# Optimization experiments

Measured on AMD Instinct MI355X. Metric: run time of the kernel, lower is better.

Reference implementation:

```python
import jax, jax.numpy as jnp
import numpy as np

B, T, D, H = 4, 2048, 1024, 16
HD = D // H  # head_dim = 64

def setup_inputs() -> dict:
    key = jax.random.key(0)
    k1, k2, k3 = jax.random.split(key, 3)
    x = jax.random.normal(k1, (B, T, D), dtype=jnp.float32)
    w_qkv = jax.random.normal(k2, (D, 3 * D), dtype=jnp.float32) * (D ** -0.5)
    b_qkv = jnp.zeros((3 * D,), dtype=jnp.float32)
    w_proj = jax.random.normal(k3, (D, D), dtype=jnp.float32) * (D ** -0.5)
    b_proj = jnp.zeros((D,), dtype=jnp.float32)
    return {"x": x, "w_qkv": w_qkv, "b_qkv": b_qkv, "w_proj": w_proj, "b_proj": b_proj}

def reference(x, w_qkv, b_qkv, w_proj, b_proj):
    b, t, d = x.shape
    scale = HD ** -0.5
    qkv = x @ w_qkv + b_qkv                          # [B,T,3D]
    qkv = qkv.reshape(b, t, 3, H, HD)
    qkv = jnp.transpose(qkv, (2, 0, 3, 1, 4))        # [3,B,H,T,HD]
    q, k, v = qkv[0], qkv[1], qkv[2]
    att = jnp.einsum("bhqd,bhkd->bhqk", q, k) * scale  # [B,H,T,T]
    mask = jnp.tril(jnp.ones((t, t), dtype=att.dtype))[None, None]
    att = att * mask + (1.0 - mask) * (-1e9)
    att = jax.nn.softmax(att, axis=-1)
    # dropout inactive (training=False)
    y = jnp.einsum("bhqk,bhkd->bhqd", att, v)        # [B,H,T,HD]
    y = jnp.transpose(y, (0, 2, 1, 3)).reshape(b, t, d)
    return y @ w_proj + b_proj
```

## Files before the change

kernel.cpp:

```cpp
#include <hip/hip_runtime.h>
#include <hip/hip_bf16.h>

typedef unsigned short u16;
typedef short short8 __attribute__((ext_vector_type(8)));
typedef short bf16x4 __attribute__((ext_vector_type(4)));
typedef float f32x4 __attribute__((ext_vector_type(4)));
typedef float f32x16 __attribute__((ext_vector_type(16)));

#define B_SZ 4
#define T_SEQ 2048
#define DMODEL 1024
#define NH 16
#define HD 64
#define QKV_ELEMS 8388608ull
#define QSCALE (0.125f * 1.44269504f)

__device__ __forceinline__ u16 f2bf(float f) {
    __hip_bfloat16 h = __float2bfloat16(f);
    return __builtin_bit_cast(u16, h);
}

__device__ __forceinline__ void gload16(const void* g, void* l) {
    __builtin_amdgcn_global_load_lds(
        (const __attribute__((address_space(1))) unsigned int*)g,
        (__attribute__((address_space(3))) unsigned int*)l, 16, 0, 0);
}

__global__ __launch_bounds__(256) void cast_x_kernel(
    const float4* __restrict__ x, u16* __restrict__ xb)
{
    const int i = blockIdx.x * 256 + threadIdx.x;
    const float4 v = x[i];
    union { u16 u[4]; uint2 d; } p;
    p.u[0] = f2bf(v.x); p.u[1] = f2bf(v.y); p.u[2] = f2bf(v.z); p.u[3] = f2bf(v.w);
    *(uint2*)(xb + (size_t)i * 4) = p.d;
}

__global__ __launch_bounds__(256) void tcast_kernel(
    const float* __restrict__ w, u16* __restrict__ wt, int K, int N)
{
    const int n = blockIdx.x * 256 + threadIdx.x;
    const int k0 = blockIdx.y * 256;
    for (int kk = 0; kk < 256; kk += 8) {
        short8 o;
#pragma unroll
        for (int e = 0; e < 8; ++e)
            o[e] = (short)f2bf(w[(size_t)(k0 + kk + e) * N + n]);
        *(short8*)&wt[(size_t)n * K + k0 + kk] = o;
    }
}

template <int EPI>
__global__ __launch_bounds__(256) void gemm_kernel(
    const u16* __restrict__ A, const u16* __restrict__ Bt,
    const float* __restrict__ bias, void* __restrict__ outp)
{
    __shared__ u16 As[128 * 64];
    __shared__ u16 Bs[128 * 64];
    const int tid = threadIdx.x;
    const int l = tid & 63;
    const int w = tid >> 6;
    const int wm = w >> 1, wn = w & 1;
    const int m0 = blockIdx.y * 128, n0 = blockIdx.x * 128;
    const int srow = l >> 3;
    const int sch  = (l & 7) ^ srow;
    const int fr = l & 15, fq = l >> 4;

    f32x4 acc[4][4] = {};

    for (int k0 = 0; k0 < 1024; k0 += 64) {
        __syncthreads();
#pragma unroll
        for (int ii = 0; ii < 4; ++ii) {
            const int row = w * 32 + ii * 8;
            gload16(&A[(size_t)(m0 + row + srow) * 1024 + k0 + sch * 8], &As[row * 64]);
            gload16(&Bt[(size_t)(n0 + row + srow) * 1024 + k0 + sch * 8], &Bs[row * 64]);
        }
        __syncthreads();
#pragma unroll
        for (int ks = 0; ks < 2; ++ks) {
            short8 af[4], bf[4];
#pragma unroll
            for (int t = 0; t < 4; ++t) {
                const int ar = wm * 64 + t * 16 + fr;
                af[t] = *(const short8*)&As[ar * 64 + (((ks * 4 + fq) ^ (l & 7)) << 3)];
                const int br = wn * 64 + t * 16 + fr;
                bf[t] = *(const short8*)&Bs[br * 64 + (((ks * 4 + fq) ^ (l & 7)) << 3)];
            }
#pragma unroll
            for (int mt = 0; mt < 4; ++mt)
#pragma unroll
                for (int nt = 0; nt < 4; ++nt)
                    acc[mt][nt] = __builtin_amdgcn_mfma_f32_16x16x32_bf16(
                        af[mt], bf[nt], acc[mt][nt], 0, 0, 0);
        }
    }

    if (EPI == 0) {
        u16* qkv = (u16*)outp;
#pragma unroll
        for (int nt = 0; nt < 4; ++nt) {
            const int n = n0 + wn * 64 + nt * 16 + fr;
            const float bs = bias[n];
            const int which = n >> 10, hh = (n >> 6) & 15, d = n & 63;
            if (which == 2) {
                u16* dst = qkv + 2 * QKV_ELEMS;
#pragma unroll
                for (int mt = 0; mt < 4; ++mt) {
                    const int m = m0 + wm * 64 + mt * 16 + fq * 4;
                    const int bb = m >> 11, t = m & 2047;
                    bf16x4 ov;
#pragma unroll
                    for (int r = 0; r < 4; ++r) ov[r] = (short)f2bf(acc[mt][nt][r] + bs);
                    *(bf16x4*)&dst[(((size_t)(bb * NH + hh)) * HD + d) * T_SEQ + t] = ov;
                }
            } else {
                const float scl = (which == 0) ? QSCALE : 1.0f;
                u16* dst = qkv + (size_t)which * QKV_ELEMS + (size_t)hh * T_SEQ * HD + d;
#pragma unroll
                for (int mt = 0; mt < 4; ++mt)
#pragma unroll
                    for (int r = 0; r < 4; ++r) {
                        const int m = m0 + wm * 64 + mt * 16 + fq * 4 + r;
                        const int bb = m >> 11, t = m & 2047;
                        dst[(size_t)bb * (NH * T_SEQ * HD) + (size_t)t * HD] =
                            f2bf((acc[mt][nt][r] + bs) * scl);
                    }
            }
        }
    } else {
        float* C = (float*)outp;
#pragma unroll
        for (int nt = 0; nt < 4; ++nt) {
            const int n = n0 + wn * 64 + nt * 16 + fr;
            const float bs = bias[n];
#pragma unroll
            for (int mt = 0; mt < 4; ++mt)
#pragma unroll
                for (int r = 0; r < 4; ++r) {
                    const int m = m0 + wm * 64 + mt * 16 + fq * 4 + r;
                    C[(size_t)m * DMODEL + n] = acc[mt][nt][r] + bs;
                }
        }
    }
}

__global__ __launch_bounds__(256, 4) void attn_kernel(
    const u16* __restrict__ q, const u16* __restrict__ k,
    const u16* __restrict__ vT, u16* __restrict__ y)
{
    __shared__ u16 Ks[2][64 * 64];
    __shared__ u16 Vs[2][64 * 64];

    static const int PI[16] = {15, 14, 13, 12, 8, 9, 10, 11, 4, 5, 6, 7, 3, 2, 1, 0};
    const int bx = blockIdx.x;
    const int qi = PI[bx >> 6];
    const int bhpos = bx & 63;
    const int hh = bhpos & 15;
    const int bb = bhpos >> 4;
    const int q0 = qi * 128;

    const size_t hbase = ((size_t)(bb * NH + hh)) * T_SEQ * HD;
    const u16* qb = q + hbase;
    const u16* kb = k + hbase;
    const u16* vTb = vT + hbase;

    const int tid = threadIdx.x;
    const int l = tid & 63;
    const int w = tid >> 6;
    const int qn = l & 31;
    const int h = l >> 5;
    const int srow = l >> 3;
    const int sch = (l & 7) ^ srow;

    u16* Qstage = &Ks[0][0];

#pragma unroll
    for (int ii = 0; ii < 4; ++ii) {
        const int row = w * 32 + ii * 8;
        gload16(&qb[(size_t)(q0 + row + srow) * HD + sch * 8], &Qstage[row * 64]);
    }
    {
        const int row = w * 16, row2 = w * 16 + 8;
        gload16(&vTb[(size_t)(row + srow) * T_SEQ + sch * 8], &Vs[0][row * 64]);
        gload16(&vTb[(size_t)(row2 + srow) * T_SEQ + sch * 8], &Vs[0][row2 * 64]);
    }
    __syncthreads();

    short8 qf[4];
    {
        const int qrow = w * 32 + qn;
#pragma unroll
        for (int k16 = 0; k16 < 4; ++k16)
            qf[k16] = *(const short8*)
                &Qstage[qrow * 64 + (((k16 * 2 + h) ^ (qrow & 7)) << 3)];
    }
    __syncthreads();

    {
        const int row = w * 16, row2 = w * 16 + 8;
        gload16(&kb[(size_t)(row + srow) * HD + sch * 8], &Ks[0][row * 64]);
        gload16(&kb[(size_t)(row2 + srow) * HD + sch * 8], &Ks[0][row2 * 64]);
    }

    const int q0w = q0 + w * 32;
    float l_run = 0.f;
    f32x16 o_acc[2] = {};

    const int nkt = 2 * (qi + 1);
    for (int kt = 0; kt < nkt; ++kt) {
        __syncthreads();
        if (kt + 1 < nkt) {
            const int nb = (kt + 1) & 1;
            const int jj = (kt + 1) * 64;
            const int row = w * 16, row2 = w * 16 + 8;
            gload16(&kb[(size_t)(jj + row + srow) * HD + sch * 8],
                    &Ks[nb][row * 64]);
            gload16(&kb[(size_t)(jj + row2 + srow) * HD + sch * 8],
                    &Ks[nb][row2 * 64]);
            gload16(&vTb[(size_t)(row + srow) * T_SEQ + jj + sch * 8],
                    &Vs[nb][row * 64]);
            gload16(&vTb[(size_t)(row2 + srow) * T_SEQ + jj + sch * 8],
                    &Vs[nb][row2 * 64]);
        }
        const int buf = kt & 1;
        const int j0 = kt * 64;

        if (j0 > q0w + 31) continue;
        const int njt = (j0 + 32 <= q0w + 31) ? 2 : 1;

        f32x16 st[2];
#pragma unroll
        for (int jt = 0; jt < 2; ++jt) {
            if (jt >= njt) continue;
            f32x16 s;
#pragma unroll
            for (int r = 0; r < 16; ++r) s[r] = -16.f;
#pragma unroll
            for (int k16 = 0; k16 < 4; ++k16) {
                const int jrow = jt * 32 + qn;
                const short8 kf = *(const short8*)
                    &Ks[buf][jrow * 64 + (((k16 * 2 + h) ^ (jrow & 7)) << 3)];
                s = __builtin_amdgcn_mfma_f32_32x32x16_bf16(kf, qf[k16], s, 0, 0, 0);
            }
            st[jt] = s;
        }

        const int qg = q0w + qn;
#pragma unroll
        for (int jt = 0; jt < 2; ++jt) {
            if (jt >= njt) continue;
            const bool needMask = (j0 + jt * 32 + 31) > q0w;
            if (needMask) {
#pragma unroll
                for (int r = 0; r < 16; ++r) {
                    const int jg = j0 + jt * 32 + (r & 3) + 8 * (r >> 2) + 4 * h;
                    if (jg > qg) st[jt][r] = -1e30f;
                }
            }
        }

        float ls = 0.f;
#pragma unroll
        for (int jt = 0; jt < 2; ++jt) {
            if (jt >= njt) continue;
            float s0 = 0.f, s1 = 0.f, s2 = 0.f, s3 = 0.f;
#pragma unroll
            for (int r = 0; r < 16; r += 4) {
                float p0 = exp2f(st[jt][r]);
                float p1 = exp2f(st[jt][r + 1]);
                float p2 = exp2f(st[jt][r + 2]);
                float p3 = exp2f(st[jt][r + 3]);
                st[jt][r] = p0; st[jt][r + 1] = p1;
                st[jt][r + 2] = p2; st[jt][r + 3] = p3;
                s0 += p0; s1 += p1; s2 += p2; s3 += p3;
            }
            ls += (s0 + s1) + (s2 + s3);
        }
        ls += __shfl_xor(ls, 32);
        l_run += ls;

#pragma unroll
        for (int jt = 0; jt < 2; ++jt) {
            if (jt >= njt) continue;
#pragma unroll
            for (int g = 0; g < 4; ++g) {
                bf16x4 pk;
#pragma unroll
                for (int e = 0; e < 4; ++e) pk[e] = (short)f2bf(st[jt][g * 4 + e]);
#pragma unroll
                for (int dt = 0; dt < 2; ++dt) {
                    const int drow = dt * 32 + qn;
                    const bf16x4 vf = *(const bf16x4*)
                        &Vs[buf][drow * 64 +
                                 (((jt * 4 + g) ^ (drow & 7)) << 3) + h * 4];
                    o_acc[dt] = __builtin_amdgcn_mfma_f32_32x32x8bf16_1k(
                        vf, pk, o_acc[dt], 0, 0, 0);
                }
            }
        }
    }

    const float inv = 1.f / l_run;
    const int t = q0w + qn;
    u16* yrow = y + ((size_t)(bb * T_SEQ + t)) * DMODEL + hh * HD;
#pragma unroll
    for (int dt = 0; dt < 2; ++dt)
#pragma unroll
        for (int g = 0; g < 4; ++g) {
            bf16x4 ov;
#pragma unroll
            for (int e = 0; e < 4; ++e)
                ov[e] = (short)f2bf(o_acc[dt][g * 4 + e] * inv);
            *(bf16x4*)&yrow[dt * 32 + g * 8 + h * 4] = ov;
        }
}

extern "C" void kernel_launch(void* const* d_in, const int* in_sizes, int n_in,
                              void* d_out, int out_size, void* d_ws, size_t ws_size,
                              hipStream_t stream) {
    const float* x      = (const float*)d_in[0];
    const float* w_qkv  = (const float*)d_in[1];
    const float* b_qkv  = (const float*)d_in[2];
    const float* w_proj = (const float*)d_in[3];
    const float* b_proj = (const float*)d_in[4];
    float* out = (float*)d_out;

    u16* xb  = (u16*)d_ws;
    u16* wqT = xb + 8388608;
    u16* wpT = wqT + 3145728;
    u16* qkv = wpT + 1048576;
    u16* yb  = qkv + 3 * QKV_ELEMS;

    cast_x_kernel<<<8192, 256, 0, stream>>>((const float4*)x, xb);
    tcast_kernel<<<dim3(12, 4), 256, 0, stream>>>(w_qkv, wqT, 1024, 3072);
    tcast_kernel<<<dim3(4, 4), 256, 0, stream>>>(w_proj, wpT, 1024, 1024);
    gemm_kernel<0><<<dim3(24, 64), 256, 0, stream>>>(xb, wqT, b_qkv, (void*)qkv);
    attn_kernel<<<dim3(1024), 256, 0, stream>>>(
        qkv, qkv + QKV_ELEMS, qkv + 2 * QKV_ELEMS, yb);
    gemm_kernel<1><<<dim3(8, 64), 256, 0, stream>>>(yb, wpT, b_proj, (void*)out);
}
```

Baseline: 326.1 us.

## Balance causal attention work by pairing short and long query tiles with split-K merge

Each attention block now takes a share of a paired short and long query tile. Part 0 computes the short tile in full and then the first half of the long tile's keys. Part 1 computes the rest of the long tile's keys. The partial outputs and row sums go to scratch buffers. An atomic flag decides which block merges them and writes the final row. The aim is to give all 1024 blocks about the same work, removing the causal tail imbalance. The cost is a memset launch, extra global traffic for the partials, and bf16 rounding of the partial outputs.

```diff
diff --git a/kernel.cpp b/kernel.cpp
--- a/kernel.cpp
+++ b/kernel.cpp
@@ -147,18 +147,19 @@
 
 __global__ __launch_bounds__(256, 4) void attn_kernel(
     const u16* __restrict__ q, const u16* __restrict__ k,
-    const u16* __restrict__ vT, u16* __restrict__ y)
+    const u16* __restrict__ vT, u16* __restrict__ y,
+    u16* __restrict__ po, float* __restrict__ pl, unsigned* __restrict__ flg)
 {
     __shared__ u16 Ks[2][64 * 64];
     __shared__ u16 Vs[2][64 * 64];
-
-    static const int PI[16] = {15, 14, 13, 12, 8, 9, 10, 11, 4, 5, 6, 7, 3, 2, 1, 0};
+    __shared__ unsigned who;
+
     const int bx = blockIdx.x;
-    const int qi = PI[bx >> 6];
-    const int bhpos = bx & 63;
-    const int hh = bhpos & 15;
-    const int bb = bhpos >> 4;
-    const int q0 = qi * 128;
+    const int part_id = bx >> 9;
+    const int pr = (bx >> 6) & 7;
+    const int hh = (bx & 7) | (((bx >> 3) & 1) << 3);
+    const int bb = (bx >> 4) & 3;
+    const int pairG = bx & 511;
 
     const size_t hbase = ((size_t)(bb * NH + hh)) * T_SEQ * HD;
     const u16* qb = q + hbase;
@@ -175,145 +176,200 @@
 
     u16* Qstage = &Ks[0][0];
 
-#pragma unroll
-    for (int ii = 0; ii < 4; ++ii) {
-        const int row = w * 32 + ii * 8;
-        gload16(&qb[(size_t)(q0 + row + srow) * HD + sch * 8], &Qstage[row * 64]);
+    auto span = [&](const int q0, const int kt0, const int ktN,
+                    f32x16 (&o_acc)[2], float& l_run) {
+        __syncthreads();
+
+#pragma unroll
+        for (int ii = 0; ii < 4; ++ii) {
+            const int row = w * 32 + ii * 8;
+            gload16(&qb[(size_t)(q0 + row + srow) * HD + sch * 8], &Qstage[row * 64]);
+        }
+        {
+            const int row = w * 16, row2 = w * 16 + 8;
+            gload16(&vTb[(size_t)(row + srow) * T_SEQ + kt0 * 64 + sch * 8],
+                    &Vs[kt0 & 1][row * 64]);
+            gload16(&vTb[(size_t)(row2 + srow) * T_SEQ + kt0 * 64 + sch * 8],
+                    &Vs[kt0 & 1][row2 * 64]);
+        }
+        __syncthreads();
+
+        short8 qf[4];
+        {
+            const int qrow = w * 32 + qn;
+#pragma unroll
+            for (int k16 = 0; k16 < 4; ++k16)
+                qf[k16] = *(const short8*)
+                    &Qstage[qrow * 64 + (((k16 * 2 + h) ^ (qrow & 7)) << 3)];
+        }
+        __syncthreads();
+
+        {
+            const int row = w * 16, row2 = w * 16 + 8;
+            gload16(&kb[(size_t)(kt0 * 64 + row + srow) * HD + sch * 8],
+                    &Ks[kt0 & 1][row * 64]);
+            gload16(&kb[(size_t)(kt0 * 64 + row2 + srow) * HD + sch * 8],
+                    &Ks[kt0 & 1][row2 * 64]);
+        }
+
+        const int q0w = q0 + w * 32;
+
+        for (int kt = kt0; kt < ktN; ++kt) {
+            __syncthreads();
+            if (kt + 1 < ktN) {
+                const int nb = (kt + 1) & 1;
+                const int jj = (kt + 1) * 64;
+                const int row = w * 16, row2 = w * 16 + 8;
+                gload16(&kb[(size_t)(jj + row + srow) * HD + sch * 8],
+                        &Ks[nb][row * 64]);
+                gload16(&kb[(size_t)(jj + row2 + srow) * HD + sch * 8],
+                        &Ks[nb][row2 * 64]);
+                gload16(&vTb[(size_t)(row + srow) * T_SEQ + jj + sch * 8],
+                        &Vs[nb][row * 64]);
+                gload16(&vTb[(size_t)(row2 + srow) * T_SEQ + jj + sch * 8],
+                        &Vs[nb][row2 * 64]);
+            }
+            const int buf = kt & 1;
+            const int j0 = kt * 64;
+
+            if (j0 > q0w + 31) continue;
+            const int njt = (j0 + 32 <= q0w + 31) ? 2 : 1;
+
+            f32x16 st[2];
+#pragma unroll
+            for (int jt = 0; jt < 2; ++jt) {
+                if (jt >= njt) continue;
+                f32x16 s;
+#pragma unroll
+                for (int r = 0; r < 16; ++r) s[r] = -16.f;
+#pragma unroll
+                for (int k16 = 0; k16 < 4; ++k16) {
+                    const int jrow = jt * 32 + qn;
+                    const short8 kf = *(const short8*)
+                        &Ks[buf][jrow * 64 + (((k16 * 2 + h) ^ (jrow & 7)) << 3)];
+                    s = __builtin_amdgcn_mfma_f32_32x32x16_bf16(kf, qf[k16], s, 0, 0, 0);
+                }
+                st[jt] = s;
+            }
+
+            const int qg = q0w + qn;
+#pragma unroll
+            for (int jt = 0; jt < 2; ++jt) {
+                if (jt >= njt) continue;
+                const bool needMask = (j0 + jt * 32 + 31) > q0w;
+                if (needMask) {
+#pragma unroll
+                    for (int r = 0; r < 16; ++r) {
+                        const int jg = j0 + jt * 32 + (r & 3) + 8 * (r >> 2) + 4 * h;
+                        if (jg > qg) st[jt][r] = -1e30f;
+                    }
+                }
+            }
+
+            float ls = 0.f;
+#pragma unroll
+            for (int jt = 0; jt < 2; ++jt) {
+                if (jt >= njt) continue;
+                float s0 = 0.f, s1 = 0.f, s2 = 0.f, s3 = 0.f;
+#pragma unroll
+                for (int r = 0; r < 16; r += 4) {
+                    float p0 = exp2f(st[jt][r]);
+                    float p1 = exp2f(st[jt][r + 1]);
+                    float p2 = exp2f(st[jt][r + 2]);
+                    float p3 = exp2f(st[jt][r + 3]);
+                    st[jt][r] = p0; st[jt][r + 1] = p1;
+                    st[jt][r + 2] = p2; st[jt][r + 3] = p3;
+                    s0 += p0; s1 += p1; s2 += p2; s3 += p3;
+                }
+                ls += (s0 + s1) + (s2 + s3);
+            }
+            ls += __shfl_xor(ls, 32);
+            l_run += ls;
+
+#pragma unroll
+            for (int jt = 0; jt < 2; ++jt) {
+                if (jt >= njt) continue;
+#pragma unroll
+                for (int g = 0; g < 4; ++g) {
+                    bf16x4 pk;
+#pragma unroll
+                    for (int e = 0; e < 4; ++e) pk[e] = (short)f2bf(st[jt][g * 4 + e]);
+#pragma unroll
+                    for (int dt = 0; dt < 2; ++dt) {
+                        const int drow = dt * 32 + qn;
+                        const bf16x4 vf = *(const bf16x4*)
+                            &Vs[buf][drow * 64 +
+                                     (((jt * 4 + g) ^ (drow & 7)) << 3) + h * 4];
+                        o_acc[dt] = __builtin_amdgcn_mfma_f32_32x32x8bf16_1k(
+                            vf, pk, o_acc[dt], 0, 0, 0);
+                    }
+                }
+            }
+        }
+    };
+
+    auto writeY = [&](const int q0, f32x16 (&o)[2], const float lt) {
+        const float inv = 1.f / lt;
+        const int t = q0 + w * 32 + qn;
+        u16* yrow = y + ((size_t)(bb * T_SEQ + t)) * DMODEL + hh * HD;
+#pragma unroll
+        for (int dt = 0; dt < 2; ++dt)
+#pragma unroll
+            for (int g = 0; g < 4; ++g) {
+                bf16x4 ov;
+#pragma unroll
+                for (int e = 0; e < 4; ++e)
+                    ov[e] = (short)f2bf(o[dt][g * 4 + e] * inv);
+                *(bf16x4*)&yrow[dt * 32 + g * 8 + h * 4] = ov;
+            }
+    };
+
+    const int qip = 15 - pr;
+    f32x16 ob[2] = {};
+    float lb = 0.f;
+
+    if (part_id == 0) {
+        f32x16 oa[2] = {};
+        float la = 0.f;
+        span(pr * 128, 0, 2 * pr + 2, oa, la);
+        writeY(pr * 128, oa, la);
+        span(qip * 128, 0, 15 - 2 * pr, ob, lb);
+    } else {
+        span(qip * 128, 15 - 2 * pr, 32 - 2 * pr, ob, lb);
     }
+
     {
-        const int row = w * 16, row2 = w * 16 + 8;
-        gload16(&vTb[(size_t)(row + srow) * T_SEQ + sch * 8], &Vs[0][row * 64]);
-        gload16(&vTb[(size_t)(row2 + srow) * T_SEQ + sch * 8], &Vs[0][row2 * 64]);
+        unsigned* s32 = (unsigned*)(po + (size_t)(pairG * 2 + part_id) * 8192);
+#pragma unroll
+        for (int dt = 0; dt < 2; ++dt)
+#pragma unroll
+            for (int r = 0; r < 16; r += 2) {
+                const unsigned pk = (unsigned)f2bf(ob[dt][r]) |
+                                    ((unsigned)f2bf(ob[dt][r + 1]) << 16);
+                s32[(dt * 8 + (r >> 1)) * 256 + tid] = pk;
+            }
+        pl[(size_t)(pairG * 2 + part_id) * 256 + tid] = lb;
+        __threadfence();
+        __syncthreads();
+        if (tid == 0) who = atomicAdd(&flg[pairG], 1u);
+        __syncthreads();
+        if (who == 1) {
+            __threadfence();
+            const unsigned* o32 = (const unsigned*)
+                (po + (size_t)(pairG * 2 + (1 - part_id)) * 8192);
+            const float lo = pl[(size_t)(pairG * 2 + (1 - part_id)) * 256 + tid];
+            const float lt = lb + lo;
+#pragma unroll
+            for (int dt = 0; dt < 2; ++dt)
+#pragma unroll
+                for (int r = 0; r < 16; r += 2) {
+                    const unsigned v = o32[(dt * 8 + (r >> 1)) * 256 + tid];
+                    ob[dt][r]     += __builtin_bit_cast(float, v << 16);
+                    ob[dt][r + 1] += __builtin_bit_cast(float, v & 0xffff0000u);
+                }
+            writeY(qip * 128, ob, lt);
+        }
     }
-    __syncthreads();
-
-    short8 qf[4];
-    {
-        const int qrow = w * 32 + qn;
-#pragma unroll
-        for (int k16 = 0; k16 < 4; ++k16)
-            qf[k16] = *(const short8*)
-                &Qstage[qrow * 64 + (((k16 * 2 + h) ^ (qrow & 7)) << 3)];
-    }
-    __syncthreads();
-
-    {
-        const int row = w * 16, row2 = w * 16 + 8;
-        gload16(&kb[(size_t)(row + srow) * HD + sch * 8], &Ks[0][row * 64]);
-        gload16(&kb[(size_t)(row2 + srow) * HD + sch * 8], &Ks[0][row2 * 64]);
-    }
-
-    const int q0w = q0 + w * 32;
-    float l_run = 0.f;
-    f32x16 o_acc[2] = {};
-
-    const int nkt = 2 * (qi + 1);
-    for (int kt = 0; kt < nkt; ++kt) {
-        __syncthreads();
-        if (kt + 1 < nkt) {
-            const int nb = (kt + 1) & 1;
-            const int jj = (kt + 1) * 64;
-            const int row = w * 16, row2 = w * 16 + 8;
-            gload16(&kb[(size_t)(jj + row + srow) * HD + sch * 8],
-                    &Ks[nb][row * 64]);
-            gload16(&kb[(size_t)(jj + row2 + srow) * HD + sch * 8],
-                    &Ks[nb][row2 * 64]);
-            gload16(&vTb[(size_t)(row + srow) * T_SEQ + jj + sch * 8],
-                    &Vs[nb][row * 64]);
-            gload16(&vTb[(size_t)(row2 + srow) * T_SEQ + jj + sch * 8],
-                    &Vs[nb][row2 * 64]);
-        }
-        const int buf = kt & 1;
-        const int j0 = kt * 64;
-
-        if (j0 > q0w + 31) continue;
-        const int njt = (j0 + 32 <= q0w + 31) ? 2 : 1;
-
-        f32x16 st[2];
-#pragma unroll
-        for (int jt = 0; jt < 2; ++jt) {
-            if (jt >= njt) continue;
-            f32x16 s;
-#pragma unroll
-            for (int r = 0; r < 16; ++r) s[r] = -16.f;
-#pragma unroll
-            for (int k16 = 0; k16 < 4; ++k16) {
-                const int jrow = jt * 32 + qn;
-                const short8 kf = *(const short8*)
-                    &Ks[buf][jrow * 64 + (((k16 * 2 + h) ^ (jrow & 7)) << 3)];
-                s = __builtin_amdgcn_mfma_f32_32x32x16_bf16(kf, qf[k16], s, 0, 0, 0);
-            }
-            st[jt] = s;
-        }
-
-        const int qg = q0w + qn;
-#pragma unroll
-        for (int jt = 0; jt < 2; ++jt) {
-            if (jt >= njt) continue;
-            const bool needMask = (j0 + jt * 32 + 31) > q0w;
-            if (needMask) {
-#pragma unroll
-                for (int r = 0; r < 16; ++r) {
-                    const int jg = j0 + jt * 32 + (r & 3) + 8 * (r >> 2) + 4 * h;
-                    if (jg > qg) st[jt][r] = -1e30f;
-                }
-            }
-        }
-
-        float ls = 0.f;
-#pragma unroll
-        for (int jt = 0; jt < 2; ++jt) {
-            if (jt >= njt) continue;
-            float s0 = 0.f, s1 = 0.f, s2 = 0.f, s3 = 0.f;
-#pragma unroll
-            for (int r = 0; r < 16; r += 4) {
-                float p0 = exp2f(st[jt][r]);
-                float p1 = exp2f(st[jt][r + 1]);
-                float p2 = exp2f(st[jt][r + 2]);
-                float p3 = exp2f(st[jt][r + 3]);
-                st[jt][r] = p0; st[jt][r + 1] = p1;
-                st[jt][r + 2] = p2; st[jt][r + 3] = p3;
-                s0 += p0; s1 += p1; s2 += p2; s3 += p3;
-            }
-            ls += (s0 + s1) + (s2 + s3);
-        }
-        ls += __shfl_xor(ls, 32);
-        l_run += ls;
-
-#pragma unroll
-        for (int jt = 0; jt < 2; ++jt) {
-            if (jt >= njt) continue;
-#pragma unroll
-            for (int g = 0; g < 4; ++g) {
-                bf16x4 pk;
-#pragma unroll
-                for (int e = 0; e < 4; ++e) pk[e] = (short)f2bf(st[jt][g * 4 + e]);
-#pragma unroll
-                for (int dt = 0; dt < 2; ++dt) {
-                    const int drow = dt * 32 + qn;
-                    const bf16x4 vf = *(const bf16x4*)
-                        &Vs[buf][drow * 64 +
-                                 (((jt * 4 + g) ^ (drow & 7)) << 3) + h * 4];
-                    o_acc[dt] = __builtin_amdgcn_mfma_f32_32x32x8bf16_1k(
-                        vf, pk, o_acc[dt], 0, 0, 0);
-                }
-            }
-        }
-    }
-
-    const float inv = 1.f / l_run;
-    const int t = q0w + qn;
-    u16* yrow = y + ((size_t)(bb * T_SEQ + t)) * DMODEL + hh * HD;
-#pragma unroll
-    for (int dt = 0; dt < 2; ++dt)
-#pragma unroll
-        for (int g = 0; g < 4; ++g) {
-            bf16x4 ov;
-#pragma unroll
-            for (int e = 0; e < 4; ++e)
-                ov[e] = (short)f2bf(o_acc[dt][g * 4 + e] * inv);
-            *(bf16x4*)&yrow[dt * 32 + g * 8 + h * 4] = ov;
-        }
 }
 
 extern "C" void kernel_launch(void* const* d_in, const int* in_sizes, int n_in,
@@ -332,11 +388,16 @@
     u16* qkv = wpT + 1048576;
     u16* yb  = qkv + 3 * QKV_ELEMS;
 
+    u16*      po  = xb;
+    float*    plp = (float*)wqT;
+    unsigned* flg = (unsigned*)(wqT + 2097152);
+
     cast_x_kernel<<<8192, 256, 0, stream>>>((const float4*)x, xb);
     tcast_kernel<<<dim3(12, 4), 256, 0, stream>>>(w_qkv, wqT, 1024, 3072);
     tcast_kernel<<<dim3(4, 4), 256, 0, stream>>>(w_proj, wpT, 1024, 1024);
     gemm_kernel<0><<<dim3(24, 64), 256, 0, stream>>>(xb, wqT, b_qkv, (void*)qkv);
+    hipMemsetAsync((void*)flg, 0, 512 * sizeof(unsigned), stream);
     attn_kernel<<<dim3(1024), 256, 0, stream>>>(
-        qkv, qkv + QKV_ELEMS, qkv + 2 * QKV_ELEMS, yb);
+        qkv, qkv + QKV_ELEMS, qkv + 2 * QKV_ELEMS, yb, po, plp, flg);
     gemm_kernel<1><<<dim3(8, 64), 256, 0, stream>>>(yb, wpT, b_proj, (void*)out);
 }
```

Result: slower. 542.8 us (+66.4%).
